# Kernel tuning notes

Hardware: AMD Instinct MI355X
Metric: run time of the kernel (lower is better)

The kernel has to match this reference:

```python
import jax, jax.numpy as jnp
import numpy as np

N_NODES = 50000
N_RAND_EDGES = 1_600_000
IN_F = 512
HID = 64
HEADS = 8
N_CLASSES = 20
SLOPE = 0.2  # LeakyReLU negative slope


def setup_inputs() -> dict:
    key = jax.random.key(0)
    ks = jax.random.split(key, 6)
    x = jax.random.normal(ks[0], (N_NODES, IN_F), dtype=jnp.float32)
    er = jax.random.randint(ks[1], (2, N_RAND_EDGES), 0, N_NODES)
    loops = jnp.tile(jnp.arange(N_NODES), (2, 1))  # self-loops so every row of adj is nonzero
    edge_index = jnp.concatenate([er, loops], axis=1)  # [2, E]
    # Learned parameters (per SpGraphAttentionLayer: weight [in,out], alpha [1,2*out] -> stored flat)
    W1 = jax.random.normal(ks[2], (HEADS, IN_F, HID), dtype=jnp.float32) * 0.05
    a1 = jax.random.normal(ks[3], (HEADS, 2 * HID), dtype=jnp.float32) * 0.1
    W2 = jax.random.normal(ks[4], (HEADS * HID, N_CLASSES), dtype=jnp.float32) * 0.05
    a2 = jax.random.normal(ks[5], (2 * N_CLASSES,), dtype=jnp.float32) * 0.1
    return {"x": x, "W1": W1, "a1": a1, "W2": W2, "a2": a2, "edge_index": edge_index}


def _gat_layer(x, W, a, e0, e1, n):
    # h = x @ weight; edge score = alpha . [h[src], h[dst]] computed as two per-node dots
    h = x @ W  # [N, F_out]
    f = W.shape[1]
    s_src = h @ a[:f]   # [N]
    s_dst = h @ a[f:]   # [N]
    edge_e = jnp.exp(jax.nn.leaky_relu(s_src[e0] + s_dst[e1], SLOPE))  # [E]
    rowsum = jax.ops.segment_sum(edge_e, e0, num_segments=n)  # spmm(adj_e, ones)
    agg = jax.ops.segment_sum(edge_e[:, None] * h[e1], e0, num_segments=n)  # spmm(adj_e, h)
    return agg / rowsum[:, None]


def reference(x, W1, a1, W2, a2, edge_index):
    n = x.shape[0]
    e0, e1 = edge_index[0], edge_index[1]
    # layer 1: per-head GAT, elu, concat along features (dropout is identity in eval)
    heads = [jax.nn.elu(_gat_layer(x, W1[i], a1[i], e0, e1, n)) for i in range(W1.shape[0])]
    hcat = jnp.concatenate(heads, axis=1)  # [N, HEADS*HID]
    out = jax.nn.elu(_gat_layer(hcat, W2, a2, e0, e1, n))  # [N, C]
    return out
```

## Files before the change

### kernel.cpp

```cpp
#include <hip/hip_runtime.h>
#include <hip/hip_fp16.h>
#include <math.h>

#define SLOPE 0.2f

typedef short bf16x8 __attribute__((ext_vector_type(8)));
typedef float f32x4  __attribute__((ext_vector_type(4)));

static __device__ __forceinline__ float elu_f(float x){ return x > 0.f ? x : (__expf(x) - 1.f); }
static __device__ __forceinline__ float lrelu(float t){ return t > 0.f ? t : SLOPE*t; }
static __device__ __forceinline__ unsigned short f2bf_rne(float f){
    unsigned int u = __float_as_uint(f);
    unsigned int r = (u + 0x7FFFu + ((u >> 16) & 1u)) >> 16;
    return (unsigned short)r;
}
static __device__ __forceinline__ float bf2f(unsigned short h){ return __uint_as_float(((unsigned int)h) << 16); }

__global__ void __launch_bounds__(256) hist_sliced_kernel(const int* __restrict__ e0, int E, int n,
                                                          int* __restrict__ cnt){
    const int s = blockIdx.x & 7;
    const int c = blockIdx.x >> 3;
    const int K = gridDim.x >> 3;
    const int lo = (int)((long)s*n >> 3), hi = (int)((long)(s+1)*n >> 3);
    const int i0 = (int)((long)c*E/K), i1 = (int)((long)(c+1)*E/K);
    for (int i = i0 + threadIdx.x; i < i1; i += 256){
        int j = e0[i];
        if (j >= lo && j < hi) atomicAdd(&cnt[j], 1);
    }
}

__global__ void __launch_bounds__(1024) scan_kernel(const int* __restrict__ cnt, int n,
                                                    int* __restrict__ row_ptr, int* __restrict__ cursor){
    __shared__ int wtot[16];
    __shared__ int carry_sh;
    if (threadIdx.x == 0) carry_sh = 0;
    __syncthreads();
    const int lane = threadIdx.x & 63, wid = threadIdx.x >> 6;
    const int nch = (n + 1023) >> 10;
    for (int c = 0; c < nch; ++c){
        int i = (c << 10) + threadIdx.x;
        int v = (i < n) ? cnt[i] : 0;
        int val = v;
        #pragma unroll
        for (int off = 1; off < 64; off <<= 1){
            int t = __shfl_up(val, off, 64);
            if (lane >= off) val += t;
        }
        if (lane == 63) wtot[wid] = val;
        __syncthreads();
        int tot = 0, wexcl = 0;
        #pragma unroll
        for (int w = 0; w < 16; ++w){ int t = wtot[w]; tot += t; if (w < wid) wexcl += t; }
        int excl = carry_sh + wexcl + (val - v);
        if (i < n){ row_ptr[i] = excl; cursor[i] = excl; }
        __syncthreads();
        if (threadIdx.x == 0) carry_sh += tot;
        __syncthreads();
    }
    if (threadIdx.x == 0) row_ptr[n] = carry_sh;
}

__global__ void __launch_bounds__(256) scatter_sliced_kernel(const int* __restrict__ e0, const int* __restrict__ e1,
                                                             int E, int n,
                                                             int* __restrict__ cursor, int* __restrict__ sidx){
    const int s = blockIdx.x & 7;
    const int c = blockIdx.x >> 3;
    const int K = gridDim.x >> 3;
    const int lo = (int)((long)s*n >> 3), hi = (int)((long)(s+1)*n >> 3);
    const int i0 = (int)((long)c*E/K), i1 = (int)((long)(c+1)*E/K);
    for (int i = i0 + threadIdx.x; i < i1; i += 256){
        int j = e0[i];
        if (j >= lo && j < hi){
            int p = atomicAdd(&cursor[j], 1);
            sidx[p] = e1[i];
        }
    }
}

__global__ void __launch_bounds__(256) split_x_kernel(const float* __restrict__ x,
                                                      unsigned short* __restrict__ xhi,
                                                      unsigned short* __restrict__ xlo, int total4){
    int i = blockIdx.x*256 + threadIdx.x;
    if (i >= total4) return;
    float4 v = ((const float4*)x)[i];
    ushort4 h, l;
    h.x = f2bf_rne(v.x); l.x = f2bf_rne(v.x - bf2f(h.x));
    h.y = f2bf_rne(v.y); l.y = f2bf_rne(v.y - bf2f(h.y));
    h.z = f2bf_rne(v.z); l.z = f2bf_rne(v.z - bf2f(h.z));
    h.w = f2bf_rne(v.w); l.w = f2bf_rne(v.w - bf2f(h.w));
    ((ushort4*)xhi)[i] = h;
    ((ushort4*)xlo)[i] = l;
}

__global__ void __launch_bounds__(256) prep_w_kernel(const float* __restrict__ W1,
                                                     unsigned short* __restrict__ wThi,
                                                     unsigned short* __restrict__ wTlo){
    int idx = blockIdx.x*256 + threadIdx.x;
    int head = idx >> 15, rem = idx & 32767;
    int c = rem >> 9, k = rem & 511;
    float f = W1[((size_t)head << 15) + k*64 + c];
    unsigned short h = f2bf_rne(f);
    wThi[idx] = h;
    wTlo[idx] = f2bf_rne(f - bf2f(h));
}

__global__ void __launch_bounds__(256) gemm1_mfma_kernel(const unsigned short* __restrict__ xhi,
                                                         const unsigned short* __restrict__ xlo,
                                                         const unsigned short* __restrict__ wThi,
                                                         const unsigned short* __restrict__ wTlo,
                                                         const float* __restrict__ a1,
                                                         __half* __restrict__ h_g,
                                                         float* __restrict__ ssrc, float* __restrict__ sdst, int n){
    const int w = threadIdx.x >> 6, lane = threadIdx.x & 63;
    const int hb2 = blockIdx.y*2;
    const int base = blockIdx.x*128 + w*32;
    const int lr = lane & 15, lk = lane >> 4;
    f32x4 acc[2][8] = {};
    const bf16x8 zf = {0,0,0,0,0,0,0,0};
    const int r0 = base + lr, r1 = base + 16 + lr;
    const size_t ro0 = (size_t)r0*512 + lk*8;
    const size_t ro1 = (size_t)r1*512 + lk*8;
    for (int k0 = 0; k0 < 512; k0 += 32){
        bf16x8 ah[2], al[2];
        if (r0 < n){ ah[0] = *(const bf16x8*)(xhi + ro0 + k0); al[0] = *(const bf16x8*)(xlo + ro0 + k0); }
        else        { ah[0] = zf; al[0] = zf; }
        if (r1 < n){ ah[1] = *(const bf16x8*)(xhi + ro1 + k0); al[1] = *(const bf16x8*)(xlo + ro1 + k0); }
        else        { ah[1] = zf; al[1] = zf; }
        #pragma unroll
        for (int hh = 0; hh < 2; ++hh){
            const unsigned short* whp = wThi + (((size_t)(hb2+hh)) << 15) + k0 + lk*8;
            const unsigned short* wlp = wTlo + (((size_t)(hb2+hh)) << 15) + k0 + lk*8;
            #pragma unroll
            for (int ni = 0; ni < 4; ++ni){
                bf16x8 bh = *(const bf16x8*)(whp + (size_t)(ni*16 + lr)*512);
                bf16x8 bl = *(const bf16x8*)(wlp + (size_t)(ni*16 + lr)*512);
                #pragma unroll
                for (int mi = 0; mi < 2; ++mi){
                    f32x4& A = acc[mi][hh*4+ni];
                    A = __builtin_amdgcn_mfma_f32_16x16x32_bf16(ah[mi], bh, A, 0, 0, 0);
                    A = __builtin_amdgcn_mfma_f32_16x16x32_bf16(ah[mi], bl, A, 0, 0, 0);
                    A = __builtin_amdgcn_mfma_f32_16x16x32_bf16(al[mi], bh, A, 0, 0, 0);
                }
            }
        }
    }
    #pragma unroll
    for (int hh = 0; hh < 2; ++hh){
        const int head = hb2 + hh;
        float as_[4], ad_[4];
        #pragma unroll
        for (int ni = 0; ni < 4; ++ni){
            as_[ni] = a1[(size_t)head*128 + ni*16 + lr];
            ad_[ni] = a1[(size_t)head*128 + 64 + ni*16 + lr];
        }
        #pragma unroll
        for (int mi = 0; mi < 2; ++mi){
            #pragma unroll
            for (int reg = 0; reg < 4; ++reg){
                float s = 0.f, d = 0.f;
                #pragma unroll
                for (int ni = 0; ni < 4; ++ni){
                    float v = acc[mi][hh*4+ni][reg];
                    s += v*as_[ni]; d += v*ad_[ni];
                }
                s += __shfl_xor(s, 1); d += __shfl_xor(d, 1);
                s += __shfl_xor(s, 2); d += __shfl_xor(d, 2);
                s += __shfl_xor(s, 4); d += __shfl_xor(d, 4);
                s += __shfl_xor(s, 8); d += __shfl_xor(d, 8);
                const int node = base + mi*16 + lk*4 + reg;
                if (node < n){
                    #pragma unroll
                    for (int ni = 0; ni < 4; ++ni)
                        h_g[(size_t)node*512 + head*64 + ni*16 + lr] = __float2half(acc[mi][hh*4+ni][reg]);
                    if (lr == 0){
                        ssrc[(size_t)node*8 + head] = s;
                        sdst[(size_t)node*8 + head] = d;
                    }
                }
            }
        }
    }
}

__global__ void __launch_bounds__(256) agg1_kernel(const __half* __restrict__ h_g, const float* __restrict__ ssrc,
                                                   const float* __restrict__ sdst,
                                                   const int* __restrict__ row_ptr, const int* __restrict__ sidx,
                                                   __half* __restrict__ hcat, int n){
    const int w = threadIdx.x >> 6, lane = threadIdx.x & 63;
    const int node = blockIdx.x*4 + w;
    if (node >= n) return;
    const int r0 = row_ptr[node], r1 = row_ptr[node+1];
    const int h = lane >> 3;
    const float ssh = ssrc[(size_t)node*8 + h];
    float acc[8] = {};
    float wsum = 0.f;
    int e = r0;
    for (; e + 3 < r1; e += 4){
        int j0 = sidx[e], j1 = sidx[e+1], j2 = sidx[e+2], j3 = sidx[e+3];
        uint4 g0 = *(const uint4*)(h_g + (size_t)j0*512 + lane*8);
        uint4 g1 = *(const uint4*)(h_g + (size_t)j1*512 + lane*8);
        uint4 g2 = *(const uint4*)(h_g + (size_t)j2*512 + lane*8);
        uint4 g3 = *(const uint4*)(h_g + (size_t)j3*512 + lane*8);
        float s0 = sdst[(size_t)j0*8 + h], s1 = sdst[(size_t)j1*8 + h];
        float s2 = sdst[(size_t)j2*8 + h], s3 = sdst[(size_t)j3*8 + h];
        float w0 = __expf(lrelu(ssh + s0));
        float w1 = __expf(lrelu(ssh + s1));
        float w2 = __expf(lrelu(ssh + s2));
        float w3 = __expf(lrelu(ssh + s3));
        const unsigned int* u0 = &g0.x; const unsigned int* u1 = &g1.x;
        const unsigned int* u2 = &g2.x; const unsigned int* u3 = &g3.x;
        #pragma unroll
        for (int q = 0; q < 4; ++q){
            float2 f0 = __half22float2(*(const __half2*)&u0[q]);
            float2 f1 = __half22float2(*(const __half2*)&u1[q]);
            float2 f2 = __half22float2(*(const __half2*)&u2[q]);
            float2 f3 = __half22float2(*(const __half2*)&u3[q]);
            acc[2*q]   += w0*f0.x + w1*f1.x + w2*f2.x + w3*f3.x;
            acc[2*q+1] += w0*f0.y + w1*f1.y + w2*f2.y + w3*f3.y;
        }
        wsum += (w0 + w1) + (w2 + w3);
    }
    for (; e < r1; ++e){
        int j = sidx[e];
        uint4 g = *(const uint4*)(h_g + (size_t)j*512 + lane*8);
        float wg = __expf(lrelu(ssh + sdst[(size_t)j*8 + h]));
        const unsigned int* u = &g.x;
        #pragma unroll
        for (int q = 0; q < 4; ++q){
            float2 f = __half22float2(*(const __half2*)&u[q]);
            acc[2*q]   += wg*f.x;
            acc[2*q+1] += wg*f.y;
        }
        wsum += wg;
    }
    float inv = 1.f / wsum;
    union { uint4 u; __half hv[8]; } pk;
    #pragma unroll
    for (int q = 0; q < 8; ++q) pk.hv[q] = __float2half(elu_f(acc[q]*inv));
    *(uint4*)(hcat + (size_t)node*512 + lane*8) = pk.u;
}

__global__ void __launch_bounds__(256) gemm2_kernel(const __half* __restrict__ hcat, const float* __restrict__ W2,
                                                    const float* __restrict__ a2,
                                                    float* __restrict__ h2, float* __restrict__ ssrc,
                                                    float* __restrict__ sdst, int n){
    __shared__ float As[16][257];
    __shared__ float Ws[16][20];
    const int tid = threadIdx.x;
    const int node = blockIdx.x*256 + tid;
    float acc[20] = {};
    for (int k0 = 0; k0 < 512; k0 += 16){
        uint4 u0 = {0,0,0,0}, u1 = {0,0,0,0};
        if (node < n){
            const __half* src = hcat + (size_t)node*512 + k0;
            u0 = *(const uint4*)src;
            u1 = *(const uint4*)(src + 8);
        }
        const unsigned int* ua = &u0.x;
        const unsigned int* ub = &u1.x;
        #pragma unroll
        for (int q = 0; q < 4; ++q){
            float2 f = __half22float2(*(const __half2*)&ua[q]);
            As[2*q][tid] = f.x; As[2*q+1][tid] = f.y;
            float2 g = __half22float2(*(const __half2*)&ub[q]);
            As[8+2*q][tid] = g.x; As[8+2*q+1][tid] = g.y;
        }
        for (int q = tid; q < 320; q += 256){
            int kr = q/20, cc = q%20;
            Ws[kr][cc] = W2[(size_t)(k0 + kr)*20 + cc];
        }
        __syncthreads();
        #pragma unroll
        for (int kk = 0; kk < 16; ++kk){
            float a = As[kk][tid];
            #pragma unroll
            for (int cc = 0; cc < 20; ++cc) acc[cc] += a*Ws[kk][cc];
        }
        __syncthreads();
    }
    if (node < n){
        float s0 = 0.f, s1 = 0.f;
        #pragma unroll
        for (int cc = 0; cc < 20; ++cc){
            h2[(size_t)node*20 + cc] = acc[cc];
            s0 += acc[cc]*a2[cc];
            s1 += acc[cc]*a2[20 + cc];
        }
        ssrc[node] = s0; sdst[node] = s1;
    }
}

__global__ void __launch_bounds__(256) agg2_kernel(const float* __restrict__ h2, const float* __restrict__ ssrc,
                                                   const float* __restrict__ sdstv,
                                                   const int* __restrict__ row_ptr, const int* __restrict__ sidx,
                                                   float* __restrict__ out, int n){
    const int w = threadIdx.x >> 6, lane = threadIdx.x & 63;
    const int node = blockIdx.x*4 + w;
    if (node >= n) return;
    const int r0 = row_ptr[node], r1 = row_ptr[node+1];
    const float ss = ssrc[node];
    const bool act = lane < 20;
    float acc = 0.f, wsum = 0.f;
    int e = r0;
    for (; e + 3 < r1; e += 4){
        int j0 = sidx[e], j1 = sidx[e+1], j2 = sidx[e+2], j3 = sidx[e+3];
        float v0 = act ? h2[(size_t)j0*20 + lane] : 0.f;
        float v1 = act ? h2[(size_t)j1*20 + lane] : 0.f;
        float v2 = act ? h2[(size_t)j2*20 + lane] : 0.f;
        float v3 = act ? h2[(size_t)j3*20 + lane] : 0.f;
        float s0 = sdstv[j0], s1 = sdstv[j1], s2 = sdstv[j2], s3 = sdstv[j3];
        float w0 = __expf(lrelu(ss + s0));
        float w1 = __expf(lrelu(ss + s1));
        float w2 = __expf(lrelu(ss + s2));
        float w3 = __expf(lrelu(ss + s3));
        acc += w0*v0 + w1*v1 + w2*v2 + w3*v3;
        wsum += (w0 + w1) + (w2 + w3);
    }
    for (; e < r1; ++e){
        int j = sidx[e];
        float v = act ? h2[(size_t)j*20 + lane] : 0.f;
        float wg = __expf(lrelu(ss + sdstv[j]));
        acc += wg*v; wsum += wg;
    }
    if (act) out[(size_t)node*20 + lane] = elu_f(acc / wsum);
}

extern "C" void kernel_launch(void* const* d_in, const int* in_sizes, int n_in,
                              void* d_out, int out_size, void* d_ws, size_t ws_size,
                              hipStream_t stream){
    const float* x  = (const float*)d_in[0];
    const float* W1 = (const float*)d_in[1];
    const float* a1 = (const float*)d_in[2];
    const float* W2 = (const float*)d_in[3];
    const float* a2 = (const float*)d_in[4];
    const int*   ei = (const int*)d_in[5];
    const int n = in_sizes[0] / 512;
    const int E = in_sizes[5] / 2;
    const int* e0 = ei;
    const int* e1 = ei + E;

    char* p = (char*)d_ws;
    auto alloc = [&](size_t bytes)->char*{ char* r = p; p += (bytes + 255) & ~(size_t)255; return r; };
    unsigned short* xhi  = (unsigned short*)alloc((size_t)n*512*2);
    unsigned short* xlo  = (unsigned short*)alloc((size_t)n*512*2);
    __half*         h_g  = (__half*)        alloc((size_t)n*512*2);
    unsigned short* wThi = (unsigned short*)alloc((size_t)8*64*512*2);
    unsigned short* wTlo = (unsigned short*)alloc((size_t)8*64*512*2);
    float* ssrc1   = (float*)alloc((size_t)n*8*4);
    float* sdst1   = (float*)alloc((size_t)n*8*4);
    int*   cnt     = (int*)  alloc((size_t)n*4);
    int*   row_ptr = (int*)  alloc(((size_t)n + 1)*4);
    int*   cursor  = (int*)  alloc((size_t)n*4);
    int*   sidx    = (int*)  alloc((size_t)E*4);
    __half* hcat  = (__half*)xhi;
    float*  h2    = (float*)xlo;
    float*  ssrc2 = h2 + (size_t)n*20;
    float*  sdst2 = ssrc2 + n;

    hipMemsetAsync(cnt, 0, (size_t)n*4, stream);
    const int KCH = 192;
    hist_sliced_kernel   <<<KCH*8, 256, 0, stream>>>(e0, E, n, cnt);
    scan_kernel          <<<1, 1024, 0, stream>>>(cnt, n, row_ptr, cursor);
    scatter_sliced_kernel<<<KCH*8, 256, 0, stream>>>(e0, e1, E, n, cursor, sidx);

    const int total4 = n*512/4;
    split_x_kernel<<<(total4 + 255)/256, 256, 0, stream>>>(x, xhi, xlo, total4);
    prep_w_kernel <<<1024, 256, 0, stream>>>(W1, wThi, wTlo);

    const int mb = (n + 127)/128;
    gemm1_mfma_kernel<<<dim3(mb, 4), 256, 0, stream>>>(xhi, xlo, wThi, wTlo, a1, h_g, ssrc1, sdst1, n);
    agg1_kernel      <<<(n + 3)/4,   256, 0, stream>>>(h_g, ssrc1, sdst1, row_ptr, sidx, hcat, n);

    const int nb256 = (n + 255)/256;
    gemm2_kernel<<<nb256, 256, 0, stream>>>(hcat, W2, a2, h2, ssrc2, sdst2, n);
    agg2_kernel <<<(n + 3)/4, 256, 0, stream>>>(h2, ssrc2, sdst2, row_ptr, sidx, (float*)d_out, n);
}
```

Before: 1.027 ms.

## Stage gemm1 tiles in LDS via async global-to-LDS copies and XCD remapping

```diff
diff --git a/kernel.cpp b/kernel.cpp
--- a/kernel.cpp
+++ b/kernel.cpp
@@ -15,6 +15,10 @@
     return (unsigned short)r;
 }
 static __device__ __forceinline__ float bf2f(unsigned short h){ return __uint_as_float(((unsigned int)h) << 16); }
+
+#define ASYNC_COPY16(gp, lp) \
+    __builtin_amdgcn_global_load_lds((const __attribute__((address_space(1))) void*)(gp), \
+                                     (__attribute__((address_space(3))) void*)(lp), 16, 0, 0)
 
 __global__ void __launch_bounds__(256) hist_sliced_kernel(const int* __restrict__ e0, int E, int n,
                                                           int* __restrict__ cnt){
@@ -110,72 +114,97 @@
                                                          const unsigned short* __restrict__ wTlo,
                                                          const float* __restrict__ a1,
                                                          __half* __restrict__ h_g,
-                                                         float* __restrict__ ssrc, float* __restrict__ sdst, int n){
+                                                         float* __restrict__ ssrc, float* __restrict__ sdst,
+                                                         int n, int nwg){
+    __shared__ unsigned short lds[16384];
+    const int bid = blockIdx.x;
+    const int xcd = bid & 7, jj = bid >> 3;
+    const int q = nwg >> 3, r = nwg & 7;
+    const int logical = (xcd < r ? xcd*(q+1) : r*(q+1) + (xcd-r)*q) + jj;
+    const int rowtile = logical >> 2, ct = logical & 3;
+    const int row0 = rowtile*128, col0 = ct*128;
     const int w = threadIdx.x >> 6, lane = threadIdx.x & 63;
-    const int hb2 = blockIdx.y*2;
-    const int base = blockIdx.x*128 + w*32;
+    const int wm = w >> 1, wn = w & 1;
     const int lr = lane & 15, lk = lane >> 4;
-    f32x4 acc[2][8] = {};
-    const bf16x8 zf = {0,0,0,0,0,0,0,0};
-    const int r0 = base + lr, r1 = base + 16 + lr;
-    const size_t ro0 = (size_t)r0*512 + lk*8;
-    const size_t ro1 = (size_t)r1*512 + lk*8;
+    f32x4 acc[4][4] = {};
+    const unsigned short* sbase[8];
+    unsigned int soff[8];
+    #pragma unroll
+    for (int i = 0; i < 8; ++i){
+        unsigned int off = w*8192u + i*1024u + lane*16u;
+        unsigned int arr = off >> 13, within = off & 8191u;
+        unsigned int rrow = within >> 6, kel = (within & 63u) >> 1;
+        const unsigned short* g;
+        size_t gidx;
+        if (arr == 0)      { g = xhi;  gidx = (size_t)(row0 + rrow)*512 + kel; }
+        else if (arr == 1) { g = xlo;  gidx = (size_t)(row0 + rrow)*512 + kel; }
+        else if (arr == 2) { g = wThi; gidx = (size_t)(col0 + rrow)*512 + kel; }
+        else               { g = wTlo; gidx = (size_t)(col0 + rrow)*512 + kel; }
+        sbase[i] = g + gidx;
+        soff[i] = (w*8192u + i*1024u);
+    }
+    const unsigned short* Ahi = lds;
+    const unsigned short* Alo = lds + 4096;
+    const unsigned short* Bhi = lds + 8192;
+    const unsigned short* Blo = lds + 12288;
     for (int k0 = 0; k0 < 512; k0 += 32){
-        bf16x8 ah[2], al[2];
-        if (r0 < n){ ah[0] = *(const bf16x8*)(xhi + ro0 + k0); al[0] = *(const bf16x8*)(xlo + ro0 + k0); }
-        else        { ah[0] = zf; al[0] = zf; }
-        if (r1 < n){ ah[1] = *(const bf16x8*)(xhi + ro1 + k0); al[1] = *(const bf16x8*)(xlo + ro1 + k0); }
-        else        { ah[1] = zf; al[1] = zf; }
-        #pragma unroll
-        for (int hh = 0; hh < 2; ++hh){
-            const unsigned short* whp = wThi + (((size_t)(hb2+hh)) << 15) + k0 + lk*8;
-            const unsigned short* wlp = wTlo + (((size_t)(hb2+hh)) << 15) + k0 + lk*8;
+        #pragma unroll
+        for (int i = 0; i < 8; ++i)
+            ASYNC_COPY16(sbase[i] + k0, (char*)lds + soff[i]);
+        __syncthreads();
+        bf16x8 a_h[4], a_l[4], b_h[4], b_l[4];
+        #pragma unroll
+        for (int mi = 0; mi < 4; ++mi){
+            int rowl = wm*64 + mi*16 + lr;
+            a_h[mi] = *(const bf16x8*)(Ahi + rowl*32 + lk*8);
+            a_l[mi] = *(const bf16x8*)(Alo + rowl*32 + lk*8);
+        }
+        #pragma unroll
+        for (int ni = 0; ni < 4; ++ni){
+            int coll = wn*64 + ni*16 + lr;
+            b_h[ni] = *(const bf16x8*)(Bhi + coll*32 + lk*8);
+            b_l[ni] = *(const bf16x8*)(Blo + coll*32 + lk*8);
+        }
+        #pragma unroll
+        for (int mi = 0; mi < 4; ++mi)
             #pragma unroll
             for (int ni = 0; ni < 4; ++ni){
-                bf16x8 bh = *(const bf16x8*)(whp + (size_t)(ni*16 + lr)*512);
-                bf16x8 bl = *(const bf16x8*)(wlp + (size_t)(ni*16 + lr)*512);
+                f32x4& A = acc[mi][ni];
+                A = __builtin_amdgcn_mfma_f32_16x16x32_bf16(a_h[mi], b_h[ni], A, 0, 0, 0);
+                A = __builtin_amdgcn_mfma_f32_16x16x32_bf16(a_h[mi], b_l[ni], A, 0, 0, 0);
+                A = __builtin_amdgcn_mfma_f32_16x16x32_bf16(a_l[mi], b_h[ni], A, 0, 0, 0);
+            }
+        __syncthreads();
+    }
+    const int head = ct*2 + wn;
+    float as_[4], ad_[4];
+    #pragma unroll
+    for (int ni = 0; ni < 4; ++ni){
+        as_[ni] = a1[(size_t)head*128 + ni*16 + lr];
+        ad_[ni] = a1[(size_t)head*128 + 64 + ni*16 + lr];
+    }
+    #pragma unroll
+    for (int mi = 0; mi < 4; ++mi){
+        #pragma unroll
+        for (int reg = 0; reg < 4; ++reg){
+            float s = 0.f, d = 0.f;
+            #pragma unroll
+            for (int ni = 0; ni < 4; ++ni){
+                float v = acc[mi][ni][reg];
+                s += v*as_[ni]; d += v*ad_[ni];
+            }
+            s += __shfl_xor(s, 1); d += __shfl_xor(d, 1);
+            s += __shfl_xor(s, 2); d += __shfl_xor(d, 2);
+            s += __shfl_xor(s, 4); d += __shfl_xor(d, 4);
+            s += __shfl_xor(s, 8); d += __shfl_xor(d, 8);
+            const int node = row0 + wm*64 + mi*16 + lk*4 + reg;
+            if (node < n){
                 #pragma unroll
-                for (int mi = 0; mi < 2; ++mi){
-                    f32x4& A = acc[mi][hh*4+ni];
-                    A = __builtin_amdgcn_mfma_f32_16x16x32_bf16(ah[mi], bh, A, 0, 0, 0);
-                    A = __builtin_amdgcn_mfma_f32_16x16x32_bf16(ah[mi], bl, A, 0, 0, 0);
-                    A = __builtin_amdgcn_mfma_f32_16x16x32_bf16(al[mi], bh, A, 0, 0, 0);
-                }
-            }
-        }
-    }
-    #pragma unroll
-    for (int hh = 0; hh < 2; ++hh){
-        const int head = hb2 + hh;
-        float as_[4], ad_[4];
-        #pragma unroll
-        for (int ni = 0; ni < 4; ++ni){
-            as_[ni] = a1[(size_t)head*128 + ni*16 + lr];
-            ad_[ni] = a1[(size_t)head*128 + 64 + ni*16 + lr];
-        }
-        #pragma unroll
-        for (int mi = 0; mi < 2; ++mi){
-            #pragma unroll
-            for (int reg = 0; reg < 4; ++reg){
-                float s = 0.f, d = 0.f;
-                #pragma unroll
-                for (int ni = 0; ni < 4; ++ni){
-                    float v = acc[mi][hh*4+ni][reg];
-                    s += v*as_[ni]; d += v*ad_[ni];
-                }
-                s += __shfl_xor(s, 1); d += __shfl_xor(d, 1);
-                s += __shfl_xor(s, 2); d += __shfl_xor(d, 2);
-                s += __shfl_xor(s, 4); d += __shfl_xor(d, 4);
-                s += __shfl_xor(s, 8); d += __shfl_xor(d, 8);
-                const int node = base + mi*16 + lk*4 + reg;
-                if (node < n){
-                    #pragma unroll
-                    for (int ni = 0; ni < 4; ++ni)
-                        h_g[(size_t)node*512 + head*64 + ni*16 + lr] = __float2half(acc[mi][hh*4+ni][reg]);
-                    if (lr == 0){
-                        ssrc[(size_t)node*8 + head] = s;
-                        sdst[(size_t)node*8 + head] = d;
-                    }
+                for (int ni = 0; ni < 4; ++ni)
+                    h_g[(size_t)node*512 + head*64 + ni*16 + lr] = __float2half(acc[mi][ni][reg]);
+                if (lr == 0){
+                    ssrc[(size_t)node*8 + head] = s;
+                    sdst[(size_t)node*8 + head] = d;
                 }
             }
         }
@@ -368,8 +397,9 @@
     prep_w_kernel <<<1024, 256, 0, stream>>>(W1, wThi, wTlo);
 
     const int mb = (n + 127)/128;
-    gemm1_mfma_kernel<<<dim3(mb, 4), 256, 0, stream>>>(xhi, xlo, wThi, wTlo, a1, h_g, ssrc1, sdst1, n);
-    agg1_kernel      <<<(n + 3)/4,   256, 0, stream>>>(h_g, ssrc1, sdst1, row_ptr, sidx, hcat, n);
+    const int nwg = mb*4;
+    gemm1_mfma_kernel<<<nwg, 256, 0, stream>>>(xhi, xlo, wThi, wTlo, a1, h_g, ssrc1, sdst1, n, nwg);
+    agg1_kernel      <<<(n + 3)/4, 256, 0, stream>>>(h_g, ssrc1, sdst1, row_ptr, sidx, hcat, n);
 
     const int nb256 = (n + 255)/256;
     gemm2_kernel<<<nb256, 256, 0, stream>>>(hcat, W2, a2, h2, ssrc2, sdst2, n);
```

Measured after the change: 869.8 us. 15.3% less time.
